# Kernel tuning notes

Hardware: AMD Instinct MI355X
Metric: run time of the kernel (lower is better)

## Reference

```python
import jax, jax.numpy as jnp
import numpy as np

B, T, C = 1, 4096, 1024
NH, NKV, HD = 16, 4, 64
N_REP = NH // NKV
WIN = 1024
EPS = 1e-5
ROPE_THETA = 10000.0


def setup_inputs() -> dict:
    key = jax.random.key(0)
    ks = jax.random.split(key, 6)
    s = 1.0 / np.sqrt(C)
    x = jax.random.normal(ks[0], (B, T, C), jnp.float32)
    wq = jax.random.normal(ks[1], (NH * HD, C), jnp.float32) * s
    wk = jax.random.normal(ks[2], (NKV * HD, C), jnp.float32) * s
    wv = jax.random.normal(ks[3], (NKV * HD, C), jnp.float32) * s
    wo = jax.random.normal(ks[4], (C, NH * HD), jnp.float32) * (1.0 / np.sqrt(NH * HD))
    q_norm_w = jnp.ones((HD,), jnp.float32)
    k_norm_w = jnp.ones((HD,), jnp.float32)
    # RoPE tables: (T, HD//2)
    inv_freq = 1.0 / (ROPE_THETA ** (np.arange(0, HD, 2, dtype=np.float32) / HD))
    ang = np.outer(np.arange(T, dtype=np.float32), inv_freq)
    freqs_cos = jnp.asarray(np.cos(ang), jnp.float32)
    freqs_sin = jnp.asarray(np.sin(ang), jnp.float32)
    return {"x": x, "wq": wq, "wk": wk, "wv": wv, "wo": wo,
            "q_norm_w": q_norm_w, "k_norm_w": k_norm_w,
            "freqs_cos": freqs_cos, "freqs_sin": freqs_sin}


def _rmsnorm(v, w):
    # RMSNorm over last dim (per-head)
    return v * jax.lax.rsqrt(jnp.mean(v * v, axis=-1, keepdims=True) + EPS) * w


def _rope(v, cos, sin):
    # v: (B, T, H, HD); interleaved complex rotation, matching torch polar freqs_cis
    vr, vi = v[..., 0::2], v[..., 1::2]
    c = cos[None, :, None, :]
    s = sin[None, :, None, :]
    out_r = vr * c - vi * s
    out_i = vr * s + vi * c
    return jnp.stack([out_r, out_i], axis=-1).reshape(v.shape)


def reference(x, wq, wk, wv, wo, q_norm_w, k_norm_w, freqs_cos, freqs_sin):
    xq = jnp.einsum('btc,dc->btd', x, wq).reshape(B, T, NH, HD)
    xk = jnp.einsum('btc,dc->btd', x, wk).reshape(B, T, NKV, HD)
    xv = jnp.einsum('btc,dc->btd', x, wv).reshape(B, T, NKV, HD)
    # per-head QK RMSNorm
    xq = _rmsnorm(xq, q_norm_w)
    xk = _rmsnorm(xk, k_norm_w)
    # RoPE
    xq = _rope(xq, freqs_cos, freqs_sin)
    xk = _rope(xk, freqs_cos, freqs_sin)
    # GQA: expand kv heads
    xk = jnp.repeat(xk, N_REP, axis=2)  # (B, T, NH, HD)
    xv = jnp.repeat(xv, N_REP, axis=2)
    scale = 1.0 / np.sqrt(HD)
    scores = jnp.einsum('bthd,bshd->bhts', xq, xk) * scale
    i = jnp.arange(T)[:, None]
    j = jnp.arange(T)[None, :]
    mask = (i >= j) & (i - j < WIN)  # causal + sliding window
    scores = jnp.where(mask[None, None], scores, -jnp.inf)
    attn = jax.nn.softmax(scores, axis=-1)
    y = jnp.einsum('bhts,bshd->bthd', attn, xv).reshape(B, T, NH * HD)
    return jnp.einsum('btd,cd->btc', y, wo)
```

## Files before the change

### kernel.cpp

```cpp
#include <hip/hip_runtime.h>
#include <hip/hip_bf16.h>


#define WIN_SZ 1024

typedef __attribute__((ext_vector_type(8))) short short8;
typedef __attribute__((ext_vector_type(8))) unsigned short ushort8;
typedef __attribute__((ext_vector_type(4))) float f32x4;
typedef __attribute__((ext_vector_type(16))) float f32x16;

#define GLOAD_LDS16(g, s)                                              \
  __builtin_amdgcn_global_load_lds(                                    \
      (const __attribute__((address_space(1))) unsigned int*)(g),      \
      (__attribute__((address_space(3))) unsigned int*)(s), 16, 0, 0)

__device__ __forceinline__ unsigned short f2bf(float f) {
  union { float f; unsigned u; } v; v.f = f;
  unsigned r = v.u + 0x7fffu + ((v.u >> 16) & 1u);
  return (unsigned short)(r >> 16);
}

__device__ __forceinline__ float bf2f(unsigned short b) {
  union { unsigned u; float f; } v; v.u = ((unsigned)b) << 16; return v.f;
}

__device__ __forceinline__ unsigned pk2bf(float lo, float hi) {
  __hip_bfloat162 h = __float22bfloat162_rn(make_float2(lo, hi));
  union { __hip_bfloat162 h; unsigned u; } c; c.h = h; return c.u;
}

__device__ __forceinline__ short8 frag4(unsigned w0, unsigned w1, unsigned w2, unsigned w3) {
  union { unsigned u[4]; short8 s; } x;
  x.u[0] = w0; x.u[1] = w1; x.u[2] = w2; x.u[3] = w3; return x.s;
}

__global__ __launch_bounds__(256) void k_f2b_all(const float* __restrict__ x,
                                                 const float* __restrict__ wq,
                                                 const float* __restrict__ wk,
                                                 const float* __restrict__ wv,
                                                 const float* __restrict__ wo,
                                                 unsigned short* __restrict__ xb,
                                                 unsigned short* __restrict__ wqkvb,
                                                 unsigned short* __restrict__ wob) {
  int q = blockIdx.x * 256 + threadIdx.x;
  const float* src;
  unsigned short* dst;
  int off;
  if (q < 1048576) { src = x; dst = xb; off = q; }
  else if (q < 1310720) { src = wq; dst = wqkvb; off = q - 1048576; }
  else if (q < 1376256) { src = wk; dst = wqkvb + 1024 * 1024; off = q - 1310720; }
  else if (q < 1441792) { src = wv; dst = wqkvb + 1280 * 1024; off = q - 1376256; }
  else { src = wo; dst = wob; off = q - 1441792; }
  float4 v = ((const float4*)src)[off];
  ushort4 o;
  o.x = f2bf(v.x); o.y = f2bf(v.y); o.z = f2bf(v.z); o.w = f2bf(v.w);
  ((ushort4*)dst)[off] = o;
}

template <int BF16OUT>
__global__ __launch_bounds__(256) void k_gemmN64(const unsigned short* __restrict__ A,
                                                 const unsigned short* __restrict__ B,
                                                 void* __restrict__ Cv,
                                                 int M, int N, int K, int nblk) {
  __shared__ unsigned short As[2][128 * 64];
  __shared__ unsigned short Bs[2][64 * 64];
  const int id = blockIdx.x;
  const int chunk = gridDim.x >> 3;
  const int swz = (id & 7) * chunk + (id >> 3);
  const int n_idx = swz % nblk, m_idx = swz / nblk;
  const int m0 = m_idx * 128, n0 = n_idx * 64;

  const int tid = threadIdx.x;
  const int w = tid >> 6, l = tid & 63;
  const int wr = w >> 1, wc = w & 1;
  const int r = l & 15, g = l >> 4;
  const int lr = l >> 3, lc = l & 7;
  const int srowb = w * 32, browb = w * 16;

  f32x4 acc[4][2];
#pragma unroll
  for (int i = 0; i < 4; i++)
#pragma unroll
    for (int j = 0; j < 2; j++) acc[i][j] = {0.f, 0.f, 0.f, 0.f};

  const unsigned short* Ag = A + (size_t)(m0 + srowb + lr) * K + lc * 8;
  const unsigned short* Bg = B + (size_t)(n0 + browb + lr) * K + lc * 8;

  auto stage = [&](int buf, int k0) {
#pragma unroll
    for (int it = 0; it < 4; it++)
      GLOAD_LDS16(Ag + (size_t)(it * 8) * K + k0, &As[buf][(srowb + it * 8) * 64]);
#pragma unroll
    for (int it = 0; it < 2; it++)
      GLOAD_LDS16(Bg + (size_t)(it * 8) * K + k0, &Bs[buf][(browb + it * 8) * 64]);
  };

  stage(0, 0);
  __syncthreads();
  int cur = 0;
  const int NT = K >> 6;
  for (int t = 0; t < NT; ++t) {
    if (t + 1 < NT) stage(cur ^ 1, (t + 1) << 6);
    const char* Ab = (const char*)As[cur];
    const char* Bb = (const char*)Bs[cur];
#pragma unroll
    for (int kk = 0; kk < 2; kk++) {
      short8 af[4], bfr[2];
#pragma unroll
      for (int mi = 0; mi < 4; mi++)
        af[mi] = *(const short8*)(Ab + (wr * 64 + mi * 16 + r) * 128 + kk * 64 + g * 16);
#pragma unroll
      for (int nj = 0; nj < 2; nj++)
        bfr[nj] = *(const short8*)(Bb + (wc * 32 + nj * 16 + r) * 128 + kk * 64 + g * 16);
#pragma unroll
      for (int mi = 0; mi < 4; mi++)
#pragma unroll
        for (int nj = 0; nj < 2; nj++)
          acc[mi][nj] = __builtin_amdgcn_mfma_f32_16x16x32_bf16(af[mi], bfr[nj], acc[mi][nj], 0, 0, 0);
    }
    __syncthreads();
    cur ^= 1;
  }

#pragma unroll
  for (int mi = 0; mi < 4; mi++)
#pragma unroll
    for (int nj = 0; nj < 2; nj++) {
      int row = m0 + wr * 64 + mi * 16 + g * 4;
      int col = n0 + wc * 32 + nj * 16 + r;
      if (BF16OUT) {
        unsigned short* C = (unsigned short*)Cv;
#pragma unroll
        for (int e = 0; e < 4; e++)
          C[(size_t)(row + e) * N + col] = f2bf(acc[mi][nj][e]);
      } else {
        float* C = (float*)Cv;
#pragma unroll
        for (int e = 0; e < 4; e++)
          C[(size_t)(row + e) * N + col] = acc[mi][nj][e];
      }
    }
}

__global__ __launch_bounds__(256) void k_normrope(const unsigned short* __restrict__ QKV,
                                                  const float* __restrict__ qw,
                                                  const float* __restrict__ kw,
                                                  const float* __restrict__ fc,
                                                  const float* __restrict__ fs,
                                                  unsigned short* __restrict__ Qb,
                                                  unsigned short* __restrict__ Kb,
                                                  unsigned short* __restrict__ Vtg) {
  int gid = blockIdx.x * 4 + (threadIdx.x >> 6);
  int l = threadIdx.x & 63;
  int t = gid / 24;
  int u = gid - t * 24;
  if (u < 16) {
    float v = bf2f(QKV[(size_t)t * 1536 + u * 64 + l]);
    float ss = v * v;
#pragma unroll
    for (int off = 32; off; off >>= 1) ss += __shfl_xor(ss, off);
    float rms = rsqrtf(ss * (1.0f / 64.0f) + 1e-5f);
    float vn = v * rms * qw[l];
    float c = fc[t * 32 + (l >> 1)], s = fs[t * 32 + (l >> 1)];
    float p = __shfl_xor(vn, 1);
    float out = (l & 1) ? (p * s + vn * c) : (vn * c - p * s);
    Qb[(size_t)t * 1024 + u * 64 + l] = f2bf(out * 0.1803368801111204f);
  } else if (u < 20) {
    int hh = u - 16;
    float v = bf2f(QKV[(size_t)t * 1536 + 1024 + hh * 64 + l]);
    float ss = v * v;
#pragma unroll
    for (int off = 32; off; off >>= 1) ss += __shfl_xor(ss, off);
    float rms = rsqrtf(ss * (1.0f / 64.0f) + 1e-5f);
    float vn = v * rms * kw[l];
    float c = fc[t * 32 + (l >> 1)], s = fs[t * 32 + (l >> 1)];
    float p = __shfl_xor(vn, 1);
    float out = (l & 1) ? (p * s + vn * c) : (vn * c - p * s);
    Kb[(size_t)t * 256 + hh * 64 + l] = f2bf(out);
  } else {
    int hh = u - 20;
    Vtg[(size_t)(hh * 64 + l) * 4096 + t] = QKV[(size_t)t * 1536 + 1280 + hh * 64 + l];
  }
}

__global__ __launch_bounds__(512, 4) void k_attn6(const unsigned short* __restrict__ Qb,
                                                  const unsigned short* __restrict__ Kb,
                                                  const unsigned short* __restrict__ Vtg,
                                                  unsigned short* __restrict__ Yb) {
  __shared__ char smem[65536 + 1024];
  char* stage = smem;
  float* Obuf = (float*)smem;
  float* ml = (float*)(smem + 65536);

  const int id = blockIdx.x;
  const int cupair = id & 255, sel = id >> 8;
  int qi = cupair >> 1;
  if (sel) qi = 127 - qi;
  const int hk = (cupair & 1) * 2 + sel;
  const int q0 = qi * 32;

  const int tid = threadIdx.x, w = tid >> 6, l = tid & 63;
  const int hh = w & 3, half = w >> 2;
  const int h = hk * 4 + hh;
  const int l31 = l & 31, hi = l >> 5, l15 = l & 15;
  const int qrow = q0 + l31;

  int jlo = q0 - (WIN_SZ - 1);
  if (jlo < 0) jlo = 0;
  jlo &= ~63;
  const int jlast = ((q0 + 31) >> 6) << 6;
  const int nt = ((jlast - jlo) >> 6) + 1;
  const int nh0 = (nt + 1) >> 1;

  const int sb = tid >> 7;
  const int su = tid & 127;
  const int srow = su >> 1;
  const int sg = (su & 1) * 4;
  const int sbase = sb * 8192 + (srow & 31) * 256;
  const int srx = (srow & 15) << 4;
  const int srh = (srow >> 5) * 128;
  const bool isV = sb & 1;
  const unsigned short* gK = Kb + (size_t)srow * 256 + hk * 64 + sg * 8;
  const unsigned short* gV = Vtg + (size_t)(hk * 64 + srow) * 4096 + sg * 8;

  short8 qf[4];
#pragma unroll
  for (int ks = 0; ks < 4; ks++)
    qf[ks] = *(const short8*)(Qb + (size_t)qrow * 1024 + h * 64 + ks * 16 + hi * 8);

  f32x16 accO0, accO1;
#pragma unroll
  for (int i = 0; i < 16; i++) { accO0[i] = 0.f; accO1[i] = 0.f; }
  float m = -1e30f, lsum = 0.f;

  ushort8 pre[4];
  auto prefetch = [&](int s) {
    int jt0 = jlo + (s << 6);
    int t1 = nh0 + s;
    int jt1 = (t1 < nt) ? (jlo + (t1 << 6)) : jlo;
    int jt = (sb >= 2) ? jt1 : jt0;
    if (!isV) {
      const unsigned short* g = gK + (size_t)jt * 256;
#pragma unroll
      for (int e = 0; e < 4; e++) pre[e] = *(const ushort8*)(g + e * 8);
    } else {
      const unsigned short* g = gV + jt;
#pragma unroll
      for (int e = 0; e < 4; e++) pre[e] = *(const ushort8*)(g + e * 8);
    }
  };
  auto store_set = [&](int set) {
    char* dstb = stage + set * 32768 + sbase;
#pragma unroll
    for (int e = 0; e < 4; e++)
      *(ushort8*)(dstb + ((srh + (sg + e) * 16) ^ srx)) = pre[e];
  };

  prefetch(0);
  store_set(0);
  if (nh0 > 1) prefetch(1);
  __syncthreads();

  for (int s = 0; s < nh0; ++s) {
    if (s + 1 < nh0) {
      store_set((s + 1) & 1);
      if (s + 2 < nh0) prefetch(s + 2);
    }
    const int setoff = (s & 1) * 32768;
    const int kbase = setoff + half * 16384;
    const int vbase = kbase + 8192;

    const int myt = half ? (nh0 + s) : s;
    if (myt < nt) {
      const int jt = jlo + (myt << 6);

      f32x16 st0, st1;
#pragma unroll
      for (int i = 0; i < 16; i++) { st0[i] = 0.f; st1[i] = 0.f; }
      __builtin_amdgcn_s_setprio(1);
#pragma unroll
      for (int ks = 0; ks < 4; ks++) {
        int colb = ks * 32 + hi * 16;
        short8 kf0 = *(const short8*)(stage + kbase + l31 * 256 + (colb ^ (l15 << 4)));
        st0 = __builtin_amdgcn_mfma_f32_32x32x16_bf16(kf0, qf[ks], st0, 0, 0, 0);
        short8 kf1 = *(const short8*)(stage + kbase + l31 * 256 + ((128 + colb) ^ (l15 << 4)));
        st1 = __builtin_amdgcn_mfma_f32_32x32x16_bf16(kf1, qf[ks], st1, 0, 0, 0);
      }
      __builtin_amdgcn_s_setprio(0);

      if (jt + 63 > q0 || (q0 + 31) - jt >= WIN_SZ) {
        const int jb = jt + hi * 4;
#pragma unroll
        for (int rg = 0; rg < 16; rg++) {
          int j0 = jb + (rg & 3) + 8 * (rg >> 2);
          if (!((j0 <= qrow) && (qrow - j0 < WIN_SZ))) st0[rg] = -3.0e38f;
          int j1 = j0 + 32;
          if (!((j1 <= qrow) && (qrow - j1 < WIN_SZ))) st1[rg] = -3.0e38f;
        }
      }

      float mx = st0[0];
#pragma unroll
      for (int rg = 1; rg < 16; rg++) mx = fmaxf(mx, st0[rg]);
#pragma unroll
      for (int rg = 0; rg < 16; rg++) mx = fmaxf(mx, st1[rg]);
      mx = fmaxf(mx, __shfl_xor(mx, 32));
      if (!__all(mx <= m + 8.0f)) {
        float mnew = fmaxf(m, mx);
        float alpha = exp2f(m - mnew);
#pragma unroll
        for (int rg = 0; rg < 16; rg++) { accO0[rg] *= alpha; accO1[rg] *= alpha; }
        lsum *= alpha;
        m = mnew;
      }
      float ps = 0.f;
#pragma unroll
      for (int rg = 0; rg < 16; rg++) { st0[rg] = exp2f(st0[rg] - m); ps += st0[rg]; }
#pragma unroll
      for (int rg = 0; rg < 16; rg++) { st1[rg] = exp2f(st1[rg] - m); ps += st1[rg]; }
      lsum += ps;

      unsigned pd0[2][4], pd1[2][4];
#pragma unroll
      for (int b = 0; b < 4; b++) {
        pd0[0][b] = pk2bf(st0[4 * b], st0[4 * b + 1]);
        pd1[0][b] = pk2bf(st0[4 * b + 2], st0[4 * b + 3]);
        pd0[1][b] = pk2bf(st1[4 * b], st1[4 * b + 1]);
        pd1[1][b] = pk2bf(st1[4 * b + 2], st1[4 * b + 3]);
      }

      __builtin_amdgcn_s_setprio(1);
#pragma unroll
      for (int jj = 0; jj < 2; jj++) {
#pragma unroll
        for (int ks2 = 0; ks2 < 2; ks2++) {
          unsigned a0 = pd0[jj][2 * ks2], a1 = pd0[jj][2 * ks2 + 1];
          unsigned b0 = pd1[jj][2 * ks2], b1 = pd1[jj][2 * ks2 + 1];
          unsigned a0x = __shfl_xor(a0, 32), a1x = __shfl_xor(a1, 32);
          unsigned b0x = __shfl_xor(b0, 32), b1x = __shfl_xor(b1, 32);
          unsigned w0 = hi ? a1x : a0;
          unsigned w1 = hi ? b1x : b0;
          unsigned w2 = hi ? a1 : a0x;
          unsigned w3 = hi ? b1 : b0x;
          short8 pf = frag4(w0, w1, w2, w3);
          int colb2 = jj * 64 + ks2 * 32 + hi * 16;
          short8 vf0 = *(const short8*)(stage + vbase + l31 * 256 + (colb2 ^ (l15 << 4)));
          accO0 = __builtin_amdgcn_mfma_f32_32x32x16_bf16(vf0, pf, accO0, 0, 0, 0);
          short8 vf1 = *(const short8*)(stage + vbase + l31 * 256 + ((128 + colb2) ^ (l15 << 4)));
          accO1 = __builtin_amdgcn_mfma_f32_32x32x16_bf16(vf1, pf, accO1, 0, 0, 0);
        }
      }
      __builtin_amdgcn_s_setprio(0);
    }
    __syncthreads();
  }

  lsum += __shfl_xor(lsum, 32);
  if (half == 1) {
#pragma unroll
    for (int dd = 0; dd < 2; dd++) {
      const f32x16& a = dd ? accO1 : accO0;
#pragma unroll
      for (int rg = 0; rg < 16; rg++) {
        int d = dd * 32 + 8 * (rg >> 2) + 4 * hi + (rg & 3);
        Obuf[(hh * 64 + d) * 32 + l31] = a[rg];
      }
    }
    if (!hi) { ml[(hh * 2 + 0) * 32 + l31] = m; ml[(hh * 2 + 1) * 32 + l31] = lsum; }
  }
  __syncthreads();
  if (half == 0) {
    float m1 = ml[(hh * 2 + 0) * 32 + l31];
    float l1 = ml[(hh * 2 + 1) * 32 + l31];
    float ms = fmaxf(m, m1);
    float a0 = exp2f(m - ms), a1 = exp2f(m1 - ms);
    float inv = 1.0f / (lsum * a0 + l1 * a1);
    a0 *= inv; a1 *= inv;
#pragma unroll
    for (int dd = 0; dd < 2; dd++) {
      const f32x16& a = dd ? accO1 : accO0;
#pragma unroll
      for (int b = 0; b < 4; b++) {
        float o[4];
#pragma unroll
        for (int e = 0; e < 4; e++) {
          int d = dd * 32 + 8 * b + 4 * hi + e;
          o[e] = a[4 * b + e] * a0 + Obuf[(hh * 64 + d) * 32 + l31] * a1;
        }
        union { unsigned uu[2]; ushort4 v; } ov;
        ov.uu[0] = pk2bf(o[0], o[1]);
        ov.uu[1] = pk2bf(o[2], o[3]);
        *(ushort4*)(Yb + (size_t)qrow * 1024 + h * 64 + dd * 32 + b * 8 + hi * 4) = ov.v;
      }
    }
  }
}

extern "C" void kernel_launch(void* const* d_in, const int* in_sizes, int n_in,
                              void* d_out, int out_size, void* d_ws, size_t ws_size,
                              hipStream_t stream) {
  const float* x = (const float*)d_in[0];
  const float* wq = (const float*)d_in[1];
  const float* wk = (const float*)d_in[2];
  const float* wv = (const float*)d_in[3];
  const float* wo = (const float*)d_in[4];
  const float* qw = (const float*)d_in[5];
  const float* kw = (const float*)d_in[6];
  const float* fc = (const float*)d_in[7];
  const float* fs = (const float*)d_in[8];
  float* out = (float*)d_out;

  char* p = (char*)d_ws;
  auto alloc = [&](size_t b) {
    char* q = p;
    p += (b + 255) & ~(size_t)255;
    return q;
  };
  unsigned short* xb = (unsigned short*)alloc((size_t)4096 * 1024 * 2);
  unsigned short* wqkvb = (unsigned short*)alloc((size_t)1536 * 1024 * 2);
  unsigned short* wob = (unsigned short*)alloc((size_t)1024 * 1024 * 2);
  unsigned short* QKVb = (unsigned short*)alloc((size_t)4096 * 1536 * 2);
  unsigned short* Qb = (unsigned short*)alloc((size_t)4096 * 1024 * 2);
  unsigned short* Kb = (unsigned short*)alloc((size_t)4096 * 256 * 2);
  unsigned short* Vtg = (unsigned short*)alloc((size_t)256 * 4096 * 2);
  unsigned short* Yb = (unsigned short*)alloc((size_t)4096 * 1024 * 2);

  k_f2b_all<<<6656, 256, 0, stream>>>(x, wq, wk, wv, wo, xb, wqkvb, wob);
  k_gemmN64<1><<<768, 256, 0, stream>>>(xb, wqkvb, QKVb, 4096, 1536, 1024, 24);
  k_normrope<<<24576, 256, 0, stream>>>(QKVb, qw, kw, fc, fs, Qb, Kb, Vtg);
  k_attn6<<<512, 512, 0, stream>>>(Qb, Kb, Vtg, Yb);
  k_gemmN64<0><<<512, 256, 0, stream>>>(Yb, wob, out, 4096, 1024, 1024, 16);
}
```

Baseline: 121.0 us.

## Single-buffer attention LDS staging and use tree reductions for softmax max/sum

The attention kernel's LDS staging drops from double-buffered 64KB to a single 32KB buffer. Each iteration now syncs, stores the prefetched tile, syncs again, and then issues the next global prefetch. Halving LDS lets more blocks fit per CU. The cost is an extra barrier per tile and less overlap between the LDS store and compute. The row max and row sum inside the softmax also move from serial chains to tree reductions, which shortens the dependency chain.

Result: slower. 125.0 us (+3.3%).

```diff
diff --git a/kernel.cpp b/kernel.cpp
--- a/kernel.cpp
+++ b/kernel.cpp
@@ -183,14 +183,14 @@
   }
 }
 
-__global__ __launch_bounds__(512, 4) void k_attn6(const unsigned short* __restrict__ Qb,
+__global__ __launch_bounds__(512, 4) void k_attn7(const unsigned short* __restrict__ Qb,
                                                   const unsigned short* __restrict__ Kb,
                                                   const unsigned short* __restrict__ Vtg,
                                                   unsigned short* __restrict__ Yb) {
-  __shared__ char smem[65536 + 1024];
+  __shared__ char smem[4 * 8192 + 1024];
   char* stage = smem;
   float* Obuf = (float*)smem;
-  float* ml = (float*)(smem + 65536);
+  float* ml = (float*)(smem + 32768);
 
   const int id = blockIdx.x;
   const int cupair = id & 255, sel = id >> 8;
@@ -249,26 +249,20 @@
       for (int e = 0; e < 4; e++) pre[e] = *(const ushort8*)(g + e * 8);
     }
   };
-  auto store_set = [&](int set) {
-    char* dstb = stage + set * 32768 + sbase;
-#pragma unroll
-    for (int e = 0; e < 4; e++)
-      *(ushort8*)(dstb + ((srh + (sg + e) * 16) ^ srx)) = pre[e];
-  };
-
   prefetch(0);
-  store_set(0);
-  if (nh0 > 1) prefetch(1);
-  __syncthreads();
+
+  const int kbase = half * 16384;
+  const int vbase = kbase + 8192;
 
   for (int s = 0; s < nh0; ++s) {
-    if (s + 1 < nh0) {
-      store_set((s + 1) & 1);
-      if (s + 2 < nh0) prefetch(s + 2);
-    }
-    const int setoff = (s & 1) * 32768;
-    const int kbase = setoff + half * 16384;
-    const int vbase = kbase + 8192;
+    __syncthreads();
+#pragma unroll
+    for (int e = 0; e < 4; e++) {
+      int dst = sbase + ((srh + (sg + e) * 16) ^ srx);
+      *(ushort8*)(stage + dst) = pre[e];
+    }
+    __syncthreads();
+    if (s + 1 < nh0) prefetch(s + 1);
 
     const int myt = half ? (nh0 + s) : s;
     if (myt < nt) {
@@ -299,12 +293,16 @@
         }
       }
 
-      float mx = st0[0];
-#pragma unroll
-      for (int rg = 1; rg < 16; rg++) mx = fmaxf(mx, st0[rg]);
-#pragma unroll
-      for (int rg = 0; rg < 16; rg++) mx = fmaxf(mx, st1[rg]);
-      mx = fmaxf(mx, __shfl_xor(mx, 32));
+      float tmax[8];
+#pragma unroll
+      for (int i = 0; i < 8; i++)
+        tmax[i] = fmaxf(fmaxf(st0[i], st0[i + 8]), fmaxf(st1[i], st1[i + 8]));
+#pragma unroll
+      for (int off = 4; off; off >>= 1)
+#pragma unroll
+        for (int i = 0; i < off; i++) tmax[i] = fmaxf(tmax[i], tmax[i + off]);
+      float mx = fmaxf(tmax[0], __shfl_xor(tmax[0], 32));
+
       if (!__all(mx <= m + 8.0f)) {
         float mnew = fmaxf(m, mx);
         float alpha = exp2f(m - mnew);
@@ -313,12 +311,19 @@
         lsum *= alpha;
         m = mnew;
       }
-      float ps = 0.f;
-#pragma unroll
-      for (int rg = 0; rg < 16; rg++) { st0[rg] = exp2f(st0[rg] - m); ps += st0[rg]; }
-#pragma unroll
-      for (int rg = 0; rg < 16; rg++) { st1[rg] = exp2f(st1[rg] - m); ps += st1[rg]; }
-      lsum += ps;
+#pragma unroll
+      for (int rg = 0; rg < 16; rg++) st0[rg] = exp2f(st0[rg] - m);
+#pragma unroll
+      for (int rg = 0; rg < 16; rg++) st1[rg] = exp2f(st1[rg] - m);
+      float tsum[8];
+#pragma unroll
+      for (int i = 0; i < 8; i++)
+        tsum[i] = (st0[i] + st0[i + 8]) + (st1[i] + st1[i + 8]);
+#pragma unroll
+      for (int off = 4; off; off >>= 1)
+#pragma unroll
+        for (int i = 0; i < off; i++) tsum[i] += tsum[i + off];
+      lsum += tsum[0];
 
       unsigned pd0[2][4], pd1[2][4];
 #pragma unroll
@@ -352,10 +357,10 @@
       }
       __builtin_amdgcn_s_setprio(0);
     }
-    __syncthreads();
   }
 
   lsum += __shfl_xor(lsum, 32);
+  __syncthreads();
   if (half == 1) {
 #pragma unroll
     for (int dd = 0; dd < 2; dd++) {
@@ -428,6 +433,6 @@
   k_f2b_all<<<6656, 256, 0, stream>>>(x, wq, wk, wv, wo, xb, wqkvb, wob);
   k_gemmN64<1><<<768, 256, 0, stream>>>(xb, wqkvb, QKVb, 4096, 1536, 1024, 24);
   k_normrope<<<24576, 256, 0, stream>>>(QKVb, qw, kw, fc, fs, Qb, Kb, Vtg);
-  k_attn6<<<512, 512, 0, stream>>>(Qb, Kb, Vtg, Yb);
+  k_attn7<<<512, 512, 0, stream>>>(Qb, Kb, Vtg, Yb);
   k_gemmN64<0><<<512, 256, 0, stream>>>(Yb, wob, out, 4096, 1024, 1024, 16);
 }
```
